# Kernel optimization log

Measured on AMD Instinct MI355X. Metric: run time of the kernel, lower is better.

Reference implementation:

```python
import jax, jax.numpy as jnp
import numpy as np

N_NODES = 50000
N_EDGES = 25000
NNZ = 800000
IN_DIM = 256
OUT_DIM = 256


def setup_inputs() -> dict:
    key = jax.random.key(0)
    k1, k2, k3, k4, k5 = jax.random.split(key, 5)
    X = jax.random.normal(k1, (N_NODES, IN_DIM), dtype=jnp.float32)
    node_idx = jax.random.randint(k2, (NNZ,), 0, N_NODES, dtype=jnp.int64)
    edge_idx = jax.random.randint(k3, (NNZ,), 0, N_EDGES, dtype=jnp.int64)
    # Xavier-uniform-ish weight, zero bias (matches reset_parameters)
    limit = float(np.sqrt(6.0 / (IN_DIM + OUT_DIM)))
    W = jax.random.uniform(k4, (IN_DIM, OUT_DIM), dtype=jnp.float32, minval=-limit, maxval=limit)
    b = jnp.zeros((OUT_DIM,), dtype=jnp.float32)
    return {"X": X, "node_idx": node_idx, "edge_idx": edge_idx, "W": W, "b": b}


def reference(X, node_idx, edge_idx, W, b):
    # Y = X @ W + b  -- dense GEMM
    Y = X @ W + b  # [N, out_dim]

    ones = jnp.ones(node_idx.shape[0], dtype=Y.dtype)
    # D_v = rowsum(H)^-0.5 (inf -> 0); D_e = colsum(H)^-1 (inf -> 0)
    deg_v = jax.ops.segment_sum(ones, node_idx, num_segments=N_NODES)
    deg_e = jax.ops.segment_sum(ones, edge_idx, num_segments=N_EDGES)
    d_v = jnp.where(deg_v > 0, deg_v ** -0.5, 0.0)  # [N]
    d_e = jnp.where(deg_e > 0, 1.0 / deg_e, 0.0)    # [E]

    # step1 = H^T @ (D_v X): gather scaled node rows, scatter-add into edges
    Z = d_v[:, None] * Y                                   # [N, out_dim]
    step1 = jax.ops.segment_sum(Z[node_idx], edge_idx, num_segments=N_EDGES)  # [E, out_dim]
    # step2 = D_e @ step1
    step2 = d_e[:, None] * step1                           # [E, out_dim]
    # step3 = H @ step2: gather edge rows, scatter-add into nodes
    step3 = jax.ops.segment_sum(step2[edge_idx], node_idx, num_segments=N_NODES)  # [N, out_dim]
    # final = D_v @ step3
    return d_v[:, None] * step3
```

## Files before the change

kernel.cpp:

```cpp
#include <hip/hip_runtime.h>

#define N_NODES 50000
#define N_EDGES 25000
#define NNZ     800000
#define DIM     256

#define CAP_E 88
#define CAP_V 56

#define NBE 98
#define NBV 196
#define CE_COARSE 8800
#define CV_COARSE 4500
#define NNZ_PB 2048
#define P1_BLOCKS 391

#define B_A1   0
#define B_CE   0
#define B_CV   3449600
#define B_CSRE 12800000
#define B_CSRV 17200000
#define B_WT   22800000
#define B_CURV 22931072
#define B_CURE 23131072
#define B_S1B  23231072
#define B_CCUR 23331072
#define B_DV   23332248

typedef __attribute__((ext_vector_type(8))) short s8v;
typedef __attribute__((ext_vector_type(4))) float f4v;

__device__ __forceinline__ unsigned short f2bf(float f) {
    unsigned u = __float_as_uint(f);
    u = (u + 0x7FFFu + ((u >> 16) & 1u)) >> 16;
    return (unsigned short)u;
}
__device__ __forceinline__ float bf2f(unsigned short h) {
    return __uint_as_float(((unsigned)h) << 16);
}

__global__ __launch_bounds__(256) void k_prep(
        const float* __restrict__ X, const float* __restrict__ W,
        const int* __restrict__ node_idx, const int* __restrict__ edge_idx,
        unsigned short* __restrict__ Xb, unsigned short* __restrict__ WTb,
        unsigned* __restrict__ ccurE, unsigned* __restrict__ ccurV,
        unsigned* __restrict__ coarseE, unsigned* __restrict__ coarseV) {
    if (blockIdx.x < 6250) {
        size_t i = ((size_t)blockIdx.x * 256 + threadIdx.x) * 8;
        float4 p0 = *(const float4*)(X + i);
        float4 p1 = *(const float4*)(X + i + 4);
        unsigned short o[8] = {f2bf(p0.x), f2bf(p0.y), f2bf(p0.z), f2bf(p0.w),
                               f2bf(p1.x), f2bf(p1.y), f2bf(p1.z), f2bf(p1.w)};
        *(s8v*)(Xb + i) = *(const s8v*)o;
        return;
    }
    if (blockIdx.x < 6282) {
        int t = (blockIdx.x - 6250) * 256 + threadIdx.x;
        int n = t >> 5;
        int k0 = (t & 31) * 8;
        unsigned short o[8];
#pragma unroll
        for (int j = 0; j < 8; ++j) o[j] = f2bf(W[(size_t)(k0 + j) * DIM + n]);
        *(s8v*)(WTb + (size_t)n * DIM + k0) = *(const s8v*)o;
        return;
    }

    __shared__ unsigned histE[NBE], histV[NBV], baseE[NBE], baseV[NBV];
    const int tid = threadIdx.x;
    const int pb  = blockIdx.x - 6282;
    const int base = pb * NNZ_PB;

    if (tid < NBE) histE[tid] = 0;
    if (tid < NBV) histV[tid] = 0;
    __syncthreads();

    int idx0 = base + tid * 4;
    int idx1 = base + 1024 + tid * 4;
    bool ok0 = idx0 < NNZ, ok1 = idx1 < NNZ;
    int4 v0 = ok0 ? *(const int4*)(node_idx + idx0) : (int4){0,0,0,0};
    int4 e0 = ok0 ? *(const int4*)(edge_idx + idx0) : (int4){0,0,0,0};
    int4 v1 = ok1 ? *(const int4*)(node_idx + idx1) : (int4){0,0,0,0};
    int4 e1 = ok1 ? *(const int4*)(edge_idx + idx1) : (int4){0,0,0,0};
    int vv[8] = {v0.x, v0.y, v0.z, v0.w, v1.x, v1.y, v1.z, v1.w};
    int ee[8] = {e0.x, e0.y, e0.z, e0.w, e1.x, e1.y, e1.z, e1.w};

    unsigned short locE[8], locV[8];
#pragma unroll
    for (int j = 0; j < 8; ++j) {
        bool ok = (j < 4) ? ok0 : ok1;
        if (ok) {
            locE[j] = (unsigned short)atomicAdd(&histE[ee[j] >> 8], 1u);
            locV[j] = (unsigned short)atomicAdd(&histV[vv[j] >> 8], 1u);
        }
    }
    __syncthreads();
    if (tid < NBE) baseE[tid] = atomicAdd(&ccurE[tid], histE[tid]);
    if (tid < NBV) baseV[tid] = atomicAdd(&ccurV[tid], histV[tid]);
    __syncthreads();

#pragma unroll
    for (int j = 0; j < 8; ++j) {
        bool ok = (j < 4) ? ok0 : ok1;
        if (ok) {
            unsigned e = (unsigned)ee[j], v = (unsigned)vv[j];
            unsigned pe = baseE[e >> 8] + locE[j];
            if (pe < CE_COARSE)
                coarseE[(size_t)(e >> 8) * CE_COARSE + pe] = ((e & 255u) << 16) | v;
            unsigned pv = baseV[v >> 8] + locV[j];
            if (pv < CV_COARSE)
                coarseV[(size_t)(v >> 8) * CV_COARSE + pv] = ((v & 255u) << 16) | e;
        }
    }
}

__global__ __launch_bounds__(256) void k_fine(
        const unsigned* __restrict__ coarseE, const unsigned* __restrict__ coarseV,
        const unsigned* __restrict__ ccurE, const unsigned* __restrict__ ccurV,
        unsigned short* __restrict__ csrE, unsigned short* __restrict__ csrV,
        unsigned* __restrict__ cur_e, unsigned* __restrict__ cur_v,
        float* __restrict__ dv) {
    __shared__ unsigned cnt[256];
    __shared__ unsigned short slots[256 * CAP_E];
    const int tid = threadIdx.x;
    cnt[tid] = 0;
    __syncthreads();

    if (blockIdx.x < NBE) {
        int b = blockIdx.x;
        unsigned n = ccurE[b]; n = n < CE_COARSE ? n : CE_COARSE;
        const unsigned* src = coarseE + (size_t)b * CE_COARSE;
        for (unsigned i = tid; i < n; i += 256) {
            unsigned p = src[i];
            unsigned f = p >> 16, v = p & 0xFFFFu;
            unsigned pos = atomicAdd(&cnt[f], 1u);
            if (pos < CAP_E) slots[f * CAP_E + pos] = (unsigned short)v;
        }
        __syncthreads();
        int e = b * 256 + tid;
        if (e < N_EDGES) cur_e[e] = cnt[tid];
        int rows = N_EDGES - b * 256; rows = rows < 256 ? rows : 256;
        unsigned words = (unsigned)rows * (CAP_E / 2);
        unsigned* dst = (unsigned*)(csrE + (size_t)b * 256 * CAP_E);
        const unsigned* s = (const unsigned*)slots;
        for (unsigned i = tid; i < words; i += 256) dst[i] = s[i];
    } else {
        int b = blockIdx.x - NBE;
        unsigned n = ccurV[b]; n = n < CV_COARSE ? n : CV_COARSE;
        const unsigned* src = coarseV + (size_t)b * CV_COARSE;
        for (unsigned i = tid; i < n; i += 256) {
            unsigned p = src[i];
            unsigned f = p >> 16, e = p & 0xFFFFu;
            unsigned pos = atomicAdd(&cnt[f], 1u);
            if (pos < CAP_V) slots[f * CAP_V + pos] = (unsigned short)e;
        }
        __syncthreads();
        int v = b * 256 + tid;
        if (v < N_NODES) {
            unsigned c = cnt[tid];
            cur_v[v] = c;
            dv[v] = c ? __frsqrt_rn((float)c) : 0.0f;
        }
        int rows = N_NODES - b * 256; rows = rows < 256 ? rows : 256;
        unsigned words = (unsigned)rows * (CAP_V / 2);
        unsigned* dst = (unsigned*)(csrV + (size_t)b * 256 * CAP_V);
        const unsigned* s = (const unsigned*)slots;
        for (unsigned i = tid; i < words; i += 256) dst[i] = s[i];
    }
}

__global__ __launch_bounds__(256) void k_gather_edges(
        const unsigned short* __restrict__ Xb,
        const unsigned short* __restrict__ csrE,
        const unsigned* __restrict__ cur_e,
        const float* __restrict__ dv,
        unsigned short* __restrict__ A1, float* __restrict__ s1b) {
    int w = (blockIdx.x * 256 + threadIdx.x) >> 6;
    int lane = threadIdx.x & 63;
    if (w >= N_EDGES) return;
    unsigned cnt = cur_e[w]; cnt = cnt < CAP_E ? cnt : CAP_E;
    const unsigned short* lst = csrE + (size_t)w * CAP_E;
    float ax = 0.f, ay = 0.f, az = 0.f, aw = 0.f, ss = 0.f;
    unsigned j = 0;
    for (; j + 4 <= cnt; j += 4) {
        ushort4 ids = *(const ushort4*)(lst + j);
        int v0 = ids.x, v1 = ids.y, v2 = ids.z, v3 = ids.w;
        float s0 = dv[v0], s1 = dv[v1], s2 = dv[v2], s3 = dv[v3];
        ushort4 x0 = *(const ushort4*)(Xb + (size_t)v0 * DIM + lane * 4);
        ushort4 x1 = *(const ushort4*)(Xb + (size_t)v1 * DIM + lane * 4);
        ushort4 x2 = *(const ushort4*)(Xb + (size_t)v2 * DIM + lane * 4);
        ushort4 x3 = *(const ushort4*)(Xb + (size_t)v3 * DIM + lane * 4);
        ax = fmaf(s0, bf2f(x0.x), ax); ay = fmaf(s0, bf2f(x0.y), ay);
        az = fmaf(s0, bf2f(x0.z), az); aw = fmaf(s0, bf2f(x0.w), aw);
        ax = fmaf(s1, bf2f(x1.x), ax); ay = fmaf(s1, bf2f(x1.y), ay);
        az = fmaf(s1, bf2f(x1.z), az); aw = fmaf(s1, bf2f(x1.w), aw);
        ax = fmaf(s2, bf2f(x2.x), ax); ay = fmaf(s2, bf2f(x2.y), ay);
        az = fmaf(s2, bf2f(x2.z), az); aw = fmaf(s2, bf2f(x2.w), aw);
        ax = fmaf(s3, bf2f(x3.x), ax); ay = fmaf(s3, bf2f(x3.y), ay);
        az = fmaf(s3, bf2f(x3.z), az); aw = fmaf(s3, bf2f(x3.w), aw);
        ss += (s0 + s1) + (s2 + s3);
    }
    for (; j < cnt; ++j) {
        int v = lst[j];
        float s = dv[v];
        ushort4 x = *(const ushort4*)(Xb + (size_t)v * DIM + lane * 4);
        ax = fmaf(s, bf2f(x.x), ax); ay = fmaf(s, bf2f(x.y), ay);
        az = fmaf(s, bf2f(x.z), az); aw = fmaf(s, bf2f(x.w), aw);
        ss += s;
    }
    ushort4 o = {f2bf(ax), f2bf(ay), f2bf(az), f2bf(aw)};
    *(ushort4*)(A1 + (size_t)w * DIM + lane * 4) = o;
    if (lane == 0) s1b[w] = ss;
}

__global__ __launch_bounds__(256) void k_gemm_mfma(
        const unsigned short* __restrict__ A,
        const unsigned short* __restrict__ WT,
        const float* __restrict__ bias,
        const unsigned* __restrict__ cur_e,
        const float* __restrict__ s1b,
        unsigned short* __restrict__ S2) {
    const int tid  = threadIdx.x;
    const int wv   = tid >> 6;
    const int lane = tid & 63;
    const int quad = lane >> 4;
    const int l16  = lane & 15;
    const int r0   = blockIdx.x * 64;
    const int nb   = wv * 64;

    f4v acc[4][4];
#pragma unroll
    for (int mt = 0; mt < 4; ++mt)
#pragma unroll
        for (int nt = 0; nt < 4; ++nt) acc[mt][nt] = (f4v){0.f, 0.f, 0.f, 0.f};

    for (int k0 = 0; k0 < DIM; k0 += 32) {
        s8v a[4], b[4];
#pragma unroll
        for (int nt = 0; nt < 4; ++nt) {
            int n = nb + nt * 16 + l16;
            b[nt] = *(const s8v*)(WT + (size_t)n * DIM + k0 + quad * 8);
        }
#pragma unroll
        for (int mt = 0; mt < 4; ++mt) {
            int m = r0 + mt * 16 + l16;
            m = (m < N_EDGES) ? m : (N_EDGES - 1);
            a[mt] = *(const s8v*)(A + (size_t)m * DIM + k0 + quad * 8);
        }
#pragma unroll
        for (int mt = 0; mt < 4; ++mt)
#pragma unroll
            for (int nt = 0; nt < 4; ++nt)
                acc[mt][nt] = __builtin_amdgcn_mfma_f32_16x16x32_bf16(
                    a[mt], b[nt], acc[mt][nt], 0, 0, 0);
    }

    __syncthreads();

    float bv[4];
#pragma unroll
    for (int nt = 0; nt < 4; ++nt) bv[nt] = bias[nb + nt * 16 + l16];

#pragma unroll
    for (int mt = 0; mt < 4; ++mt) {
#pragma unroll
        for (int reg = 0; reg < 4; ++reg) {
            int row = r0 + mt * 16 + quad * 4 + reg;
            if (row < N_EDGES) {
                unsigned ce = cur_e[row];
                float sc = ce ? 1.0f / (float)ce : 0.0f;
                float sb = s1b[row];
#pragma unroll
                for (int nt = 0; nt < 4; ++nt) {
                    float v = sc * (acc[mt][nt][reg] + sb * bv[nt]);
                    S2[(size_t)row * DIM + nb + nt * 16 + l16] = f2bf(v);
                }
            }
        }
    }
}

__global__ __launch_bounds__(256) void k_gather_nodes(
        const unsigned short* __restrict__ S2,
        const unsigned short* __restrict__ csrV,
        const unsigned* __restrict__ cur_v,
        const float* __restrict__ dv,
        float* __restrict__ out) {
    int w = (blockIdx.x * 256 + threadIdx.x) >> 6;
    int lane = threadIdx.x & 63;
    if (w >= N_NODES) return;
    unsigned cnt = cur_v[w]; cnt = cnt < CAP_V ? cnt : CAP_V;
    const unsigned short* lst = csrV + (size_t)w * CAP_V;
    float ax = 0.f, ay = 0.f, az = 0.f, aw = 0.f;
    unsigned j = 0;
    for (; j + 4 <= cnt; j += 4) {
        ushort4 ids = *(const ushort4*)(lst + j);
        int e0 = ids.x, e1 = ids.y, e2 = ids.z, e3 = ids.w;
        ushort4 x0 = *(const ushort4*)(S2 + (size_t)e0 * DIM + lane * 4);
        ushort4 x1 = *(const ushort4*)(S2 + (size_t)e1 * DIM + lane * 4);
        ushort4 x2 = *(const ushort4*)(S2 + (size_t)e2 * DIM + lane * 4);
        ushort4 x3 = *(const ushort4*)(S2 + (size_t)e3 * DIM + lane * 4);
        ax += (bf2f(x0.x) + bf2f(x1.x)) + (bf2f(x2.x) + bf2f(x3.x));
        ay += (bf2f(x0.y) + bf2f(x1.y)) + (bf2f(x2.y) + bf2f(x3.y));
        az += (bf2f(x0.z) + bf2f(x1.z)) + (bf2f(x2.z) + bf2f(x3.z));
        aw += (bf2f(x0.w) + bf2f(x1.w)) + (bf2f(x2.w) + bf2f(x3.w));
    }
    for (; j < cnt; ++j) {
        int e = lst[j];
        ushort4 x = *(const ushort4*)(S2 + (size_t)e * DIM + lane * 4);
        ax += bf2f(x.x); ay += bf2f(x.y); az += bf2f(x.z); aw += bf2f(x.w);
    }
    float s = dv[w];
    float4 o = {s * ax, s * ay, s * az, s * aw};
    *(float4*)(out + (size_t)w * DIM + lane * 4) = o;
}

extern "C" void kernel_launch(void* const* d_in, const int* in_sizes, int n_in,
                              void* d_out, int out_size, void* d_ws, size_t ws_size,
                              hipStream_t stream) {
    (void)in_sizes; (void)n_in; (void)out_size; (void)ws_size;
    const float* X        = (const float*)d_in[0];
    const int*   node_idx = (const int*)d_in[1];
    const int*   edge_idx = (const int*)d_in[2];
    const float* W        = (const float*)d_in[3];
    const float* bias     = (const float*)d_in[4];
    float* out = (float*)d_out;
    char*  ws  = (char*)d_ws;

    unsigned short* A1      = (unsigned short*)(ws + B_A1);
    unsigned*       coarseE = (unsigned*)(ws + B_CE);
    unsigned*       coarseV = (unsigned*)(ws + B_CV);
    unsigned short* csrE    = (unsigned short*)(ws + B_CSRE);
    unsigned short* csrV    = (unsigned short*)(ws + B_CSRV);
    unsigned short* WTb     = (unsigned short*)(ws + B_WT);
    unsigned*       cur_v   = (unsigned*)(ws + B_CURV);
    unsigned*       cur_e   = (unsigned*)(ws + B_CURE);
    float*          s1b     = (float*)(ws + B_S1B);
    unsigned*       ccurE   = (unsigned*)(ws + B_CCUR);
    unsigned*       ccurV   = ccurE + NBE;
    float*          dv      = (float*)(ws + B_DV);

    unsigned short* Xb = (unsigned short*)d_out;

    hipMemsetAsync(ccurE, 0, (NBE + NBV) * sizeof(unsigned), stream);

    k_prep<<<6282 + P1_BLOCKS, 256, 0, stream>>>(X, W, node_idx, edge_idx,
                                                 Xb, WTb, ccurE, ccurV, coarseE, coarseV);
    k_fine<<<NBE + NBV, 256, 0, stream>>>(coarseE, coarseV, ccurE, ccurV,
                                          csrE, csrV, cur_e, cur_v, dv);
    k_gather_edges<<<(N_EDGES * 64 + 255) / 256, 256, 0, stream>>>(
        Xb, csrE, cur_e, dv, A1, s1b);
    k_gemm_mfma<<<(N_EDGES + 63) / 64, 256, 0, stream>>>(A1, WTb, bias, cur_e, s1b, A1);
    k_gather_nodes<<<(N_NODES * 64 + 255) / 256, 256, 0, stream>>>(
        A1, csrV, cur_v, dv, out);
}
```

Measured before the change: 271.6 us.

## Sort per-row CSR neighbor lists and unroll gathers by eight

Adds a kernel that bitonic-sorts each edge's and node's neighbor list inside one wavefront, so the later gathers read rows in ascending address order for better cache and DRAM locality. Both gather kernels also gain an 8-wide unrolled loop that issues eight row loads before accumulating, raising memory-level parallelism. The cost is an extra kernel launch plus a pass over the CSR arrays. Summation order changes, and the 8-wide loop adds register pressure.

New measurement: 312.8 us. 15.1% more time.

```diff
diff --git a/kernel.cpp b/kernel.cpp
--- a/kernel.cpp
+++ b/kernel.cpp
@@ -168,6 +168,48 @@
     }
 }
 
+__global__ __launch_bounds__(256) void k_sort(
+        unsigned short* __restrict__ csrE, unsigned short* __restrict__ csrV,
+        const unsigned* __restrict__ cur_e, const unsigned* __restrict__ cur_v) {
+    int w = (blockIdx.x * 256 + threadIdx.x) >> 6;
+    int lane = threadIdx.x & 63;
+    unsigned short* row;
+    unsigned cnt;
+    if (w < N_EDGES) {
+        cnt = cur_e[w]; cnt = cnt < CAP_E ? cnt : CAP_E;
+        row = csrE + (size_t)w * CAP_E;
+    } else {
+        int v = w - N_EDGES;
+        if (v >= N_NODES) return;
+        cnt = cur_v[v]; cnt = cnt < CAP_V ? cnt : CAP_V;
+        row = csrV + (size_t)v * CAP_V;
+    }
+    if (cnt <= 1) return;
+    unsigned a0 = (lane < (int)cnt) ? (unsigned)row[lane] : 0xFFFFu;
+    unsigned a1 = (lane + 64 < (int)cnt) ? (unsigned)row[lane + 64] : 0xFFFFu;
+
+#pragma unroll
+    for (int k = 2; k <= 128; k <<= 1) {
+        if (k == 128) {
+            unsigned lo = a0 < a1 ? a0 : a1;
+            unsigned hi = a0 < a1 ? a1 : a0;
+            a0 = lo; a1 = hi;
+        }
+#pragma unroll
+        for (int j = (k == 128 ? 32 : (k >> 1)); j > 0; j >>= 1) {
+            bool up0 = ((lane & k) == 0);
+            bool up1 = (((64 | lane) & k) == 0);
+            unsigned p0 = __shfl_xor(a0, j, 64);
+            unsigned p1 = __shfl_xor(a1, j, 64);
+            bool lower = ((lane & j) == 0);
+            a0 = (lower == up0) ? (a0 < p0 ? a0 : p0) : (a0 < p0 ? p0 : a0);
+            a1 = (lower == up1) ? (a1 < p1 ? a1 : p1) : (a1 < p1 ? p1 : a1);
+        }
+    }
+    if (lane < (int)cnt) row[lane] = (unsigned short)a0;
+    if (lane + 64 < (int)cnt) row[lane + 64] = (unsigned short)a1;
+}
+
 __global__ __launch_bounds__(256) void k_gather_edges(
         const unsigned short* __restrict__ Xb,
         const unsigned short* __restrict__ csrE,
@@ -181,6 +223,27 @@
     const unsigned short* lst = csrE + (size_t)w * CAP_E;
     float ax = 0.f, ay = 0.f, az = 0.f, aw = 0.f, ss = 0.f;
     unsigned j = 0;
+    for (; j + 8 <= cnt; j += 8) {
+        s8v idv = *(const s8v*)(lst + j);
+        int id[8];
+#pragma unroll
+        for (int q = 0; q < 8; ++q) id[q] = (unsigned short)idv[q];
+        float sc[8];
+#pragma unroll
+        for (int q = 0; q < 8; ++q) sc[q] = dv[id[q]];
+        ushort4 xr[8];
+#pragma unroll
+        for (int q = 0; q < 8; ++q)
+            xr[q] = *(const ushort4*)(Xb + (size_t)id[q] * DIM + lane * 4);
+#pragma unroll
+        for (int q = 0; q < 8; ++q) {
+            ax = fmaf(sc[q], bf2f(xr[q].x), ax);
+            ay = fmaf(sc[q], bf2f(xr[q].y), ay);
+            az = fmaf(sc[q], bf2f(xr[q].z), az);
+            aw = fmaf(sc[q], bf2f(xr[q].w), aw);
+            ss += sc[q];
+        }
+    }
     for (; j + 4 <= cnt; j += 4) {
         ushort4 ids = *(const ushort4*)(lst + j);
         int v0 = ids.x, v1 = ids.y, v2 = ids.z, v3 = ids.w;
@@ -292,6 +355,21 @@
     const unsigned short* lst = csrV + (size_t)w * CAP_V;
     float ax = 0.f, ay = 0.f, az = 0.f, aw = 0.f;
     unsigned j = 0;
+    for (; j + 8 <= cnt; j += 8) {
+        s8v idv = *(const s8v*)(lst + j);
+        int id[8];
+#pragma unroll
+        for (int q = 0; q < 8; ++q) id[q] = (unsigned short)idv[q];
+        ushort4 xr[8];
+#pragma unroll
+        for (int q = 0; q < 8; ++q)
+            xr[q] = *(const ushort4*)(S2 + (size_t)id[q] * DIM + lane * 4);
+#pragma unroll
+        for (int q = 0; q < 8; ++q) {
+            ax += bf2f(xr[q].x); ay += bf2f(xr[q].y);
+            az += bf2f(xr[q].z); aw += bf2f(xr[q].w);
+        }
+    }
     for (; j + 4 <= cnt; j += 4) {
         ushort4 ids = *(const ushort4*)(lst + j);
         int e0 = ids.x, e1 = ids.y, e2 = ids.z, e3 = ids.w;
@@ -347,6 +425,7 @@
                                                  Xb, WTb, ccurE, ccurV, coarseE, coarseV);
     k_fine<<<NBE + NBV, 256, 0, stream>>>(coarseE, coarseV, ccurE, ccurV,
                                           csrE, csrV, cur_e, cur_v, dv);
+    k_sort<<<(N_EDGES + N_NODES + 3) / 4, 256, 0, stream>>>(csrE, csrV, cur_e, cur_v);
     k_gather_edges<<<(N_EDGES * 64 + 255) / 256, 256, 0, stream>>>(
         Xb, csrE, cur_e, dv, A1, s1b);
     k_gemm_mfma<<<(N_EDGES + 63) / 64, 256, 0, stream>>>(A1, WTb, bias, cur_e, s1b, A1);
```
